# Kernel tuning notes

Hardware: AMD Instinct MI355X
Metric: run time of the kernel (lower is better)

The kernel has to match this reference:

```python
import jax, jax.numpy as jnp
import numpy as np
from jax import lax

N = 4096      # nodes
D = 256       # in_channels
H = 128       # hidden_size (cell output = 2*H = 256)
BLOCK = 128   # row-block size for the masked-max scan
THR = 0.99    # adjacency threshold on uniform A -> avg degree ~41
EPS = 1e-12


def _block_max(m, scores):
    # m: [BLOCK, N] bool, scores: [N, H] -> [BLOCK, H]
    v = jnp.where(m[:, :, None], scores[None, :, :], -jnp.inf)
    return v.max(axis=1)

_block_max = jax.checkpoint(_block_max)


def masked_max(mask, scores):
    # maxpool over neighbors, blocked over destination nodes to avoid an [N,N,H] temp
    n = mask.shape[0]
    mblk = mask.reshape(n // BLOCK, BLOCK, n)
    def body(_, m):
        return None, _block_max(m, scores)
    _, out = lax.scan(body, None, mblk)
    out = out.reshape(n, scores.shape[-1])
    # nodes with no neighbors -> 0
    return jnp.where(jnp.isneginf(out), jnp.zeros_like(out), out)


def setup_inputs() -> dict:
    key = jax.random.key(0)
    ks = jax.random.split(key, 16)
    def w(k, shape):
        fan = shape[0]
        return (jax.random.normal(k, shape, jnp.float32) / np.sqrt(fan)).astype(jnp.float32)
    D1 = 2 * H  # layer-1 input dim (= 256)
    return dict(
        x=jax.random.normal(ks[0], (N, D), jnp.float32),
        A=jax.random.uniform(ks[1], (N, N), dtype=jnp.float32),
        # layer 0 cell params
        Wp0=w(ks[2], (D, H)), bp0=jnp.zeros((H,), jnp.float32),
        Ws0=w(ks[3], (D, H)), bs0=jnp.zeros((H,), jnp.float32),
        Wn0=w(ks[4], (H, H)), bn0=jnp.zeros((H,), jnp.float32),
        # layer 1 cell params
        Wp1=w(ks[5], (D1, H)), bp1=jnp.zeros((H,), jnp.float32),
        Ws1=w(ks[6], (D1, H)), bs1=jnp.zeros((H,), jnp.float32),
        Wn1=w(ks[7], (H, H)), bn1=jnp.zeros((H,), jnp.float32),
    )


def _cell(x, mask, Wp, bp, Ws, bs, Wn, bn):
    # GraphSAGE maxpool cell: concat(self transform, neighbor maxpool transform)
    scores = jax.nn.relu(x @ Wp + bp)                 # [N, H]
    pooled = masked_max(mask, scores)                 # [N, H]
    return jnp.concatenate([x @ Ws + bs, pooled @ Wn + bn], axis=-1)  # [N, 2H]


def reference(x, A, Wp0, bp0, Ws0, bs0, Wn0, bn0, Wp1, bp1, Ws1, bs1, Wn1, bn1):
    mask = A > THR  # [N, N] bool adjacency
    for (Wp, bp, Ws, bs, Wn, bn) in ((Wp0, bp0, Ws0, bs0, Wn0, bn0),
                                     (Wp1, bp1, Ws1, bs1, Wn1, bn1)):
        x = _cell(x, mask, Wp, bp, Ws, bs, Wn, bn)
        x = jax.nn.relu(x)
        nrm = jnp.linalg.norm(x, axis=-1, keepdims=True)
        x = x / jnp.maximum(nrm, EPS)
    return x
```

## Files before the change

kernel.cpp:

```cpp
#include <hip/hip_runtime.h>

#define NN 4096
#define CAP 256
#define THRV 0.99f
#define SROWS 8

typedef __attribute__((ext_vector_type(8))) short short8v;
typedef __attribute__((ext_vector_type(4))) float f32x4;

__device__ inline unsigned short f2bf(float f) {
  unsigned u = __builtin_bit_cast(unsigned, f);
  u = (u + 0x7fffu + ((u >> 16) & 1u)) >> 16;
  return (unsigned short)u;
}
__device__ inline unsigned pkmax(unsigned a, unsigned b) {
  unsigned r;
  asm("v_pk_max_u16 %0, %1, %2" : "=v"(r) : "v"(a), "v"(b));
  return r;
}
__device__ inline uint4 max4(uint4 a, uint4 b) {
  return make_uint4(pkmax(a.x, b.x), pkmax(a.y, b.y), pkmax(a.z, b.z), pkmax(a.w, b.w));
}


__global__ __launch_bounds__(256) void k_scan(
    const float* __restrict__ A, int* __restrict__ cnt, unsigned short* __restrict__ nbr) {
  __shared__ int scnt[SROWS];
  __shared__ unsigned short snb[SROWS][CAP];
  const int tid = threadIdx.x;
  const int lane = tid & 63;
  const int r0 = blockIdx.x * SROWS;
  if (tid < SROWS) scnt[tid] = 0;
  __syncthreads();
  const float4* Arow = (const float4*)(A + (size_t)r0 * NN);
  float4 c0 = Arow[tid], c1 = Arow[tid + 256], c2 = Arow[tid + 512], c3 = Arow[tid + 768];
  for (int r = 0; r < SROWS; ++r) {
    float4 n0 = c0, n1 = c1, n2 = c2, n3 = c3;
    if (r < SROWS - 1) {
      const float4* nx = Arow + (size_t)(r + 1) * (NN / 4);
      n0 = nx[tid]; n1 = nx[tid + 256]; n2 = nx[tid + 512]; n3 = nx[tid + 768];
    }
    unsigned m = 0;
    m |= (c0.x > THRV) ? 0x1u : 0u;    m |= (c0.y > THRV) ? 0x2u : 0u;
    m |= (c0.z > THRV) ? 0x4u : 0u;    m |= (c0.w > THRV) ? 0x8u : 0u;
    m |= (c1.x > THRV) ? 0x10u : 0u;   m |= (c1.y > THRV) ? 0x20u : 0u;
    m |= (c1.z > THRV) ? 0x40u : 0u;   m |= (c1.w > THRV) ? 0x80u : 0u;
    m |= (c2.x > THRV) ? 0x100u : 0u;  m |= (c2.y > THRV) ? 0x200u : 0u;
    m |= (c2.z > THRV) ? 0x400u : 0u;  m |= (c2.w > THRV) ? 0x800u : 0u;
    m |= (c3.x > THRV) ? 0x1000u : 0u; m |= (c3.y > THRV) ? 0x2000u : 0u;
    m |= (c3.z > THRV) ? 0x4000u : 0u; m |= (c3.w > THRV) ? 0x8000u : 0u;
    int cntT = __popc(m);
    int inc = cntT;
#pragma unroll
    for (int off = 1; off < 64; off <<= 1) {
      int o = __shfl_up(inc, off, 64);
      if (lane >= off) inc += o;
    }
    int excl = inc - cntT;
    int wtot = __shfl(inc, 63, 64);
    int wbase = 0;
    if (lane == 0) wbase = atomicAdd(&scnt[r], wtot);
    wbase = __shfl(wbase, 0, 64);
    int pos = wbase + excl;
    while (m) {
      int b = __ffs(m) - 1;
      m &= m - 1;
      if (pos < CAP) snb[r][pos] = (unsigned short)(4 * tid + 1024 * (b >> 2) + (b & 3));
      ++pos;
    }
    c0 = n0; c1 = n1; c2 = n2; c3 = n3;
  }
  __syncthreads();
  if (tid < SROWS) cnt[r0 + tid] = min(scnt[tid], CAP);
  {
    ushort4* dst = (ushort4*)(nbr + (size_t)r0 * CAP);
    const ushort4* s = (const ushort4*)snb;
    dst[tid] = s[tid];
    dst[tid + 256] = s[tid + 256];
  }
}

__global__ __launch_bounds__(256) void k_gp(
    const float* __restrict__ x,
    const float* __restrict__ Wp0, const float* __restrict__ bp0,
    const float* __restrict__ Ws0, const float* __restrict__ bs0,
    const float* __restrict__ Wn0, const float* __restrict__ Wp1,
    const float* __restrict__ Ws1, const float* __restrict__ Wn1,
    unsigned short* __restrict__ scores0, float* __restrict__ S0,
    unsigned short* __restrict__ tWn0, unsigned short* __restrict__ tWp1,
    unsigned short* __restrict__ tWs1, unsigned short* __restrict__ tWn1) {
  __shared__ unsigned short smw[32768];
  const int bid = blockIdx.x;
  const int tid = threadIdx.x;

  if (bid < 128) {
    const int set = bid >> 6;
    const float* W = set ? Ws0 : Wp0;
    const float* bias = set ? bs0 : bp0;
#pragma unroll
    for (int it = 0; it < 32; ++it) {
      int e0 = it * 1024 + tid * 4;
      float4 v = *(const float4*)(W + e0);
      int k = e0 >> 7, n = e0 & 127;
      int elem = (k & 3) + 4 * ((k >> 4) & 1);
      int gg = (k >> 2) & 3;
      int kt8 = (k >> 5) * 8;
      float vv[4] = {v.x, v.y, v.z, v.w};
#pragma unroll
      for (int i = 0; i < 4; ++i) {
        int nn = n + i;
        smw[((kt8 + (nn >> 4)) << 9) + ((gg * 16 + (nn & 15)) << 3) + elem] = f2bf(vv[i]);
      }
    }
    __syncthreads();
    const int wv = tid >> 6, lane = tid & 63;
    const int g = lane >> 4, r15 = lane & 15;
    const int rb16 = (bid & 63) * 64 + wv * 16;
    const int row = rb16 + r15;
    f32x4 acc[8] = {};
#pragma unroll
    for (int ktIdx = 0; ktIdx < 8; ++ktIdx) {
      const float* xp = x + (size_t)row * 256 + ktIdx * 32 + 4 * g;
      float4 lo = *(const float4*)xp;
      float4 hi = *(const float4*)(xp + 16);
      short8v a;
      a[0] = (short)f2bf(lo.x); a[1] = (short)f2bf(lo.y);
      a[2] = (short)f2bf(lo.z); a[3] = (short)f2bf(lo.w);
      a[4] = (short)f2bf(hi.x); a[5] = (short)f2bf(hi.y);
      a[6] = (short)f2bf(hi.z); a[7] = (short)f2bf(hi.w);
#pragma unroll
      for (int nf = 0; nf < 8; ++nf) {
        uint4 bw = *(const uint4*)(smw + ((ktIdx * 8 + nf) << 9) + lane * 8);
        acc[nf] = __builtin_amdgcn_mfma_f32_16x16x32_bf16(a, __builtin_bit_cast(short8v, bw), acc[nf], 0, 0, 0);
      }
    }
#pragma unroll
    for (int nf = 0; nf < 8; ++nf) {
      int col = nf * 16 + r15;
      float bv = bias[col];
#pragma unroll
      for (int r = 0; r < 4; ++r) {
        int orow = rb16 + 4 * g + r;
        float t = acc[nf][r] + bv;
        if (set == 0) scores0[(size_t)orow * 128 + col] = f2bf(fmaxf(t, 0.f));
        else          S0[(size_t)orow * 128 + col] = t;
      }
    }
    return;
  }
  int id = bid - 128;
  const float* src; unsigned short* dst; int base;
  if (id < 16)      { src = Wn0; dst = tWn0; base = id; }
  else if (id < 48) { src = Wp1; dst = tWp1; base = id - 16; }
  else if (id < 80) { src = Ws1; dst = tWs1; base = id - 48; }
  else              { src = Wn1; dst = tWn1; base = id - 80; }
  int e0 = base * 1024 + tid * 4;
  float4 v = *(const float4*)(src + e0);
  int k = e0 >> 7, n = e0 & 127;
  float vv[4] = {v.x, v.y, v.z, v.w};
  int elem = (k & 3) + 4 * ((k >> 4) & 1);
  int gg = (k >> 2) & 3;
  int fragkt = (k >> 5) * 8;
#pragma unroll
  for (int i = 0; i < 4; ++i) {
    int nn = n + i;
    int idx = ((fragkt + (nn >> 4)) << 9) + ((gg * 16 + (nn & 15)) << 3) + elem;
    dst[idx] = f2bf(vv[i]);
  }
}

template<int LAYER>
__global__ __launch_bounds__(512) void fusedL(
    const int* __restrict__ cnt, const unsigned short* __restrict__ nbr,
    const unsigned short* __restrict__ scores_in, const float* __restrict__ S_in,
    const unsigned short* __restrict__ tWn, const float* __restrict__ bn,
    const unsigned short* __restrict__ tWp, const float* __restrict__ bp,
    const unsigned short* __restrict__ tWs, const float* __restrict__ bs,
    unsigned short* __restrict__ scores_out, float* __restrict__ S_out,
    float* __restrict__ out) {
  __shared__ int scnt[16];
  __shared__ unsigned short snb[16][CAP];
  __shared__ unsigned short pool2[16][2][136];
  __shared__ unsigned short pooled[16][136];
  __shared__ unsigned short xb[16][264];
  __shared__ float ssqs[16];
  __shared__ float ssqw[4][16];

  const int tid = threadIdx.x;
  const int wv = tid >> 6, lane = tid & 63, g = lane >> 4, r15 = lane & 15;
  const int r0 = blockIdx.x * 16;

  if (tid < 16) scnt[tid] = cnt[r0 + tid];
  {
    const ushort4* src = (const ushort4*)(nbr + (size_t)r0 * CAP);
    ushort4* dst = (ushort4*)snb;
    dst[tid] = src[tid];
    dst[tid + 512] = src[tid + 512];
  }
  __syncthreads();

  {
    const int r = tid >> 5, sub = tid & 31;
    const int h = sub >> 4, c8 = (sub & 15) * 8;
    const int c = scnt[r];
    uint4 m0 = make_uint4(0, 0, 0, 0), m1 = m0, m2 = m0, m3 = m0;
    int k = h;
    for (; k + 6 < c; k += 8) {
      int j0 = snb[r][k], j1 = snb[r][k + 2], j2 = snb[r][k + 4], j3 = snb[r][k + 6];
      uint4 a0 = *(const uint4*)(scores_in + (size_t)j0 * 128 + c8);
      uint4 a1 = *(const uint4*)(scores_in + (size_t)j1 * 128 + c8);
      uint4 a2 = *(const uint4*)(scores_in + (size_t)j2 * 128 + c8);
      uint4 a3 = *(const uint4*)(scores_in + (size_t)j3 * 128 + c8);
      m0 = max4(m0, a0); m1 = max4(m1, a1); m2 = max4(m2, a2); m3 = max4(m3, a3);
    }
    for (; k < c; k += 2)
      m0 = max4(m0, *(const uint4*)(scores_in + (size_t)snb[r][k] * 128 + c8));
    *(uint4*)&pool2[r][h][c8] = max4(max4(m0, m1), max4(m2, m3));
  }
  __syncthreads();
  if (tid < 256) {
    const int r = tid >> 4, c8 = (tid & 15) * 8;
    uint4 a = *(const uint4*)&pool2[r][0][c8];
    uint4 b = *(const uint4*)&pool2[r][1][c8];
    *(uint4*)&pooled[r][c8] = max4(a, b);
  }
  __syncthreads();

  float sv[8];
  f32x4 pacc[2] = {};
  const int srow = tid >> 4, sc8 = (tid & 15) * 8;
  if (tid < 256) {
    const float* sp = S_in + (size_t)(r0 + srow) * 128 + sc8;
    float4 sa = *(const float4*)sp;
    float4 sb = *(const float4*)(sp + 4);
    sv[0] = fmaxf(sa.x, 0.f); sv[1] = fmaxf(sa.y, 0.f);
    sv[2] = fmaxf(sa.z, 0.f); sv[3] = fmaxf(sa.w, 0.f);
    sv[4] = fmaxf(sb.x, 0.f); sv[5] = fmaxf(sb.y, 0.f);
    sv[6] = fmaxf(sb.z, 0.f); sv[7] = fmaxf(sb.w, 0.f);
    float ps = 0.f;
#pragma unroll
    for (int i = 0; i < 8; ++i) ps += sv[i] * sv[i];
#pragma unroll
    for (int off = 1; off < 16; off <<= 1) ps += __shfl_xor(ps, off, 16);
    if ((tid & 15) == 0) ssqs[srow] = ps;
  } else {
    const int wv2 = wv - 4;
#pragma unroll
    for (int kt = 0; kt < 128; kt += 32) {
      ushort4 alo = *(const ushort4*)&pooled[r15][kt + 4 * g];
      ushort4 ahi = *(const ushort4*)&pooled[r15][kt + 16 + 4 * g];
      short8v a;
      a[0] = alo.x; a[1] = alo.y; a[2] = alo.z; a[3] = alo.w;
      a[4] = ahi.x; a[5] = ahi.y; a[6] = ahi.z; a[7] = ahi.w;
#pragma unroll
      for (int f = 0; f < 2; ++f) {
        uint4 bw = *((const uint4*)(tWn + (size_t)((kt >> 5) * 8 + 2 * wv2 + f) * 512) + lane);
        pacc[f] = __builtin_amdgcn_mfma_f32_16x16x32_bf16(a, __builtin_bit_cast(short8v, bw), pacc[f], 0, 0, 0);
      }
    }
#pragma unroll
    for (int f = 0; f < 2; ++f) {
      float bv = bn[(2 * wv2 + f) * 16 + r15];
#pragma unroll
      for (int rr = 0; rr < 4; ++rr) pacc[f][rr] = fmaxf(pacc[f][rr] + bv, 0.f);
    }
#pragma unroll
    for (int rr = 0; rr < 4; ++rr) {
      float ps = pacc[0][rr] * pacc[0][rr] + pacc[1][rr] * pacc[1][rr];
#pragma unroll
      for (int off = 1; off < 16; off <<= 1) ps += __shfl_xor(ps, off, 16);
      if (r15 == 0) ssqw[wv2][4 * g + rr] = ps;
    }
  }
  __syncthreads();

  if (LAYER == 0) {
    if (tid < 256) {
      float tot = ssqs[srow] + ssqw[0][srow] + ssqw[1][srow] + ssqw[2][srow] + ssqw[3][srow];
      float sc = 1.f / fmaxf(sqrtf(tot), 1e-12f);
      unsigned short hh[8];
#pragma unroll
      for (int i = 0; i < 8; ++i) hh[i] = f2bf(sv[i] * sc);
      uint4 wvv;
      wvv.x = (unsigned)hh[0] | ((unsigned)hh[1] << 16);
      wvv.y = (unsigned)hh[2] | ((unsigned)hh[3] << 16);
      wvv.z = (unsigned)hh[4] | ((unsigned)hh[5] << 16);
      wvv.w = (unsigned)hh[6] | ((unsigned)hh[7] << 16);
      *(uint4*)&xb[srow][sc8] = wvv;
    } else {
      const int wv2 = wv - 4;
#pragma unroll
      for (int rr = 0; rr < 4; ++rr) {
        int row = 4 * g + rr;
        float tot = ssqs[row] + ssqw[0][row] + ssqw[1][row] + ssqw[2][row] + ssqw[3][row];
        float sc = 1.f / fmaxf(sqrtf(tot), 1e-12f);
#pragma unroll
        for (int f = 0; f < 2; ++f)
          xb[row][128 + (2 * wv2 + f) * 16 + r15] = f2bf(pacc[f][rr] * sc);
      }
    }
    __syncthreads();
    const int s = wv >> 2;
    const unsigned short* Wt = s ? tWs : tWp;
    const float* bb = s ? bs : bp;
    const int nf0 = (wv & 3) * 2;
    f32x4 dacc[2] = {};
#pragma unroll
    for (int kt = 0; kt < 256; kt += 32) {
      ushort4 alo = *(const ushort4*)&xb[r15][kt + 4 * g];
      ushort4 ahi = *(const ushort4*)&xb[r15][kt + 16 + 4 * g];
      short8v a;
      a[0] = alo.x; a[1] = alo.y; a[2] = alo.z; a[3] = alo.w;
      a[4] = ahi.x; a[5] = ahi.y; a[6] = ahi.z; a[7] = ahi.w;
#pragma unroll
      for (int f = 0; f < 2; ++f) {
        uint4 bw = *((const uint4*)(Wt + (size_t)((kt >> 5) * 8 + nf0 + f) * 512) + lane);
        dacc[f] = __builtin_amdgcn_mfma_f32_16x16x32_bf16(a, __builtin_bit_cast(short8v, bw), dacc[f], 0, 0, 0);
      }
    }
#pragma unroll
    for (int f = 0; f < 2; ++f) {
      int col = (nf0 + f) * 16 + r15;
      float bv = bb[col];
#pragma unroll
      for (int rr = 0; rr < 4; ++rr) {
        int grow = r0 + 4 * g + rr;
        float t = dacc[f][rr] + bv;
        if (s == 0) scores_out[(size_t)grow * 128 + col] = f2bf(fmaxf(t, 0.f));
        else        S_out[(size_t)grow * 128 + col] = t;
      }
    }
  } else {
    if (tid < 256) {
      float tot = ssqs[srow] + ssqw[0][srow] + ssqw[1][srow] + ssqw[2][srow] + ssqw[3][srow];
      float sc = 1.f / fmaxf(sqrtf(tot), 1e-12f);
      float* op = out + (size_t)(r0 + srow) * 256 + sc8;
      *(float4*)op = make_float4(sv[0] * sc, sv[1] * sc, sv[2] * sc, sv[3] * sc);
      *(float4*)(op + 4) = make_float4(sv[4] * sc, sv[5] * sc, sv[6] * sc, sv[7] * sc);
    } else {
      const int wv2 = wv - 4;
#pragma unroll
      for (int rr = 0; rr < 4; ++rr) {
        int row = 4 * g + rr;
        float tot = ssqs[row] + ssqw[0][row] + ssqw[1][row] + ssqw[2][row] + ssqw[3][row];
        float sc = 1.f / fmaxf(sqrtf(tot), 1e-12f);
#pragma unroll
        for (int f = 0; f < 2; ++f)
          out[(size_t)(r0 + row) * 256 + 128 + (2 * wv2 + f) * 16 + r15] = pacc[f][rr] * sc;
      }
    }
  }
}

extern "C" void kernel_launch(void* const* d_in, const int* in_sizes, int n_in,
                              void* d_out, int out_size, void* d_ws, size_t ws_size,
                              hipStream_t stream) {
  (void)in_sizes; (void)n_in; (void)out_size; (void)ws_size;
  const float* x   = (const float*)d_in[0];
  const float* A   = (const float*)d_in[1];
  const float* Wp0 = (const float*)d_in[2];
  const float* bp0 = (const float*)d_in[3];
  const float* Ws0 = (const float*)d_in[4];
  const float* bs0 = (const float*)d_in[5];
  const float* Wn0 = (const float*)d_in[6];
  const float* bn0 = (const float*)d_in[7];
  const float* Wp1 = (const float*)d_in[8];
  const float* bp1 = (const float*)d_in[9];
  const float* Ws1 = (const float*)d_in[10];
  const float* bs1 = (const float*)d_in[11];
  const float* Wn1 = (const float*)d_in[12];
  const float* bn1 = (const float*)d_in[13];

  char* ws = (char*)d_ws;
  auto alloc = [&](size_t bytes) { char* p = ws; ws += (bytes + 255) & ~(size_t)255; return p; };
  int* cnt             = (int*)alloc((size_t)NN * 4);
  unsigned short* nbr  = (unsigned short*)alloc((size_t)NN * CAP * 2);
  unsigned short* tWn0 = (unsigned short*)alloc(128 * 128 * 2);
  unsigned short* tWp1 = (unsigned short*)alloc(256 * 128 * 2);
  unsigned short* tWs1 = (unsigned short*)alloc(256 * 128 * 2);
  unsigned short* tWn1 = (unsigned short*)alloc(128 * 128 * 2);
  unsigned short* scores0 = (unsigned short*)alloc((size_t)NN * 128 * 2);
  unsigned short* scores1 = (unsigned short*)alloc((size_t)NN * 128 * 2);
  float* S0            = (float*)alloc((size_t)NN * 128 * 4);
  float* S1            = (float*)alloc((size_t)NN * 128 * 4);

  k_scan<<<NN / SROWS, 256, 0, stream>>>(A, cnt, nbr);
  k_gp<<<224, 256, 0, stream>>>(x, Wp0, bp0, Ws0, bs0, Wn0, Wp1, Ws1, Wn1,
                                scores0, S0, tWn0, tWp1, tWs1, tWn1);
  fusedL<0><<<NN / 16, 512, 0, stream>>>(cnt, nbr, scores0, S0,
                                         tWn0, bn0, tWp1, bp1, tWs1, bs1,
                                         scores1, S1, nullptr);
  fusedL<1><<<NN / 16, 512, 0, stream>>>(cnt, nbr, scores1, S1,
                                         tWn1, bn1, nullptr, nullptr, nullptr, nullptr,
                                         nullptr, nullptr, (float*)d_out);
}
```

Baseline: 50.78 us.

## Fuse adjacency threshold scan into layer-0 fused kernel

Removes the separate k_scan kernel and builds each block's neighbor lists directly in fusedL<0>, with 512 threads scanning the block's 16 rows of A. The neighbor list is built in shared memory and written out for reuse by layer 1. This drops one kernel launch and the round trip of neighbor lists through global memory for layer 0. The cost is that the 64MB scan of A now runs with only 256 blocks of 512 threads, so A bandwidth may be harder to saturate, and it is serialized inside the layer-0 kernel.

New measurement: 50.02 us. Within noise of the previous version (-1.5%).

```diff
diff --git a/kernel.cpp b/kernel.cpp
--- a/kernel.cpp
+++ b/kernel.cpp
@@ -3,7 +3,6 @@
 #define NN 4096
 #define CAP 256
 #define THRV 0.99f
-#define SROWS 8
 
 typedef __attribute__((ext_vector_type(8))) short short8v;
 typedef __attribute__((ext_vector_type(4))) float f32x4;
@@ -22,63 +21,6 @@
   return make_uint4(pkmax(a.x, b.x), pkmax(a.y, b.y), pkmax(a.z, b.z), pkmax(a.w, b.w));
 }
 
-
-__global__ __launch_bounds__(256) void k_scan(
-    const float* __restrict__ A, int* __restrict__ cnt, unsigned short* __restrict__ nbr) {
-  __shared__ int scnt[SROWS];
-  __shared__ unsigned short snb[SROWS][CAP];
-  const int tid = threadIdx.x;
-  const int lane = tid & 63;
-  const int r0 = blockIdx.x * SROWS;
-  if (tid < SROWS) scnt[tid] = 0;
-  __syncthreads();
-  const float4* Arow = (const float4*)(A + (size_t)r0 * NN);
-  float4 c0 = Arow[tid], c1 = Arow[tid + 256], c2 = Arow[tid + 512], c3 = Arow[tid + 768];
-  for (int r = 0; r < SROWS; ++r) {
-    float4 n0 = c0, n1 = c1, n2 = c2, n3 = c3;
-    if (r < SROWS - 1) {
-      const float4* nx = Arow + (size_t)(r + 1) * (NN / 4);
-      n0 = nx[tid]; n1 = nx[tid + 256]; n2 = nx[tid + 512]; n3 = nx[tid + 768];
-    }
-    unsigned m = 0;
-    m |= (c0.x > THRV) ? 0x1u : 0u;    m |= (c0.y > THRV) ? 0x2u : 0u;
-    m |= (c0.z > THRV) ? 0x4u : 0u;    m |= (c0.w > THRV) ? 0x8u : 0u;
-    m |= (c1.x > THRV) ? 0x10u : 0u;   m |= (c1.y > THRV) ? 0x20u : 0u;
-    m |= (c1.z > THRV) ? 0x40u : 0u;   m |= (c1.w > THRV) ? 0x80u : 0u;
-    m |= (c2.x > THRV) ? 0x100u : 0u;  m |= (c2.y > THRV) ? 0x200u : 0u;
-    m |= (c2.z > THRV) ? 0x400u : 0u;  m |= (c2.w > THRV) ? 0x800u : 0u;
-    m |= (c3.x > THRV) ? 0x1000u : 0u; m |= (c3.y > THRV) ? 0x2000u : 0u;
-    m |= (c3.z > THRV) ? 0x4000u : 0u; m |= (c3.w > THRV) ? 0x8000u : 0u;
-    int cntT = __popc(m);
-    int inc = cntT;
-#pragma unroll
-    for (int off = 1; off < 64; off <<= 1) {
-      int o = __shfl_up(inc, off, 64);
-      if (lane >= off) inc += o;
-    }
-    int excl = inc - cntT;
-    int wtot = __shfl(inc, 63, 64);
-    int wbase = 0;
-    if (lane == 0) wbase = atomicAdd(&scnt[r], wtot);
-    wbase = __shfl(wbase, 0, 64);
-    int pos = wbase + excl;
-    while (m) {
-      int b = __ffs(m) - 1;
-      m &= m - 1;
-      if (pos < CAP) snb[r][pos] = (unsigned short)(4 * tid + 1024 * (b >> 2) + (b & 3));
-      ++pos;
-    }
-    c0 = n0; c1 = n1; c2 = n2; c3 = n3;
-  }
-  __syncthreads();
-  if (tid < SROWS) cnt[r0 + tid] = min(scnt[tid], CAP);
-  {
-    ushort4* dst = (ushort4*)(nbr + (size_t)r0 * CAP);
-    const ushort4* s = (const ushort4*)snb;
-    dst[tid] = s[tid];
-    dst[tid + 256] = s[tid + 256];
-  }
-}
 
 __global__ __launch_bounds__(256) void k_gp(
     const float* __restrict__ x,
@@ -171,7 +113,8 @@
 
 template<int LAYER>
 __global__ __launch_bounds__(512) void fusedL(
-    const int* __restrict__ cnt, const unsigned short* __restrict__ nbr,
+    const float* __restrict__ A,
+    int* __restrict__ cnt, unsigned short* __restrict__ nbr,
     const unsigned short* __restrict__ scores_in, const float* __restrict__ S_in,
     const unsigned short* __restrict__ tWn, const float* __restrict__ bn,
     const unsigned short* __restrict__ tWp, const float* __restrict__ bp,
@@ -190,14 +133,62 @@
   const int wv = tid >> 6, lane = tid & 63, g = lane >> 4, r15 = lane & 15;
   const int r0 = blockIdx.x * 16;
 
-  if (tid < 16) scnt[tid] = cnt[r0 + tid];
-  {
-    const ushort4* src = (const ushort4*)(nbr + (size_t)r0 * CAP);
-    ushort4* dst = (ushort4*)snb;
-    dst[tid] = src[tid];
-    dst[tid + 512] = src[tid + 512];
-  }
-  __syncthreads();
+  if (LAYER == 0) {
+    if (tid < 16) scnt[tid] = 0;
+    __syncthreads();
+    const float4* Ar = (const float4*)(A + (size_t)r0 * NN);
+    float4 c0 = Ar[tid], c1 = Ar[tid + 512];
+    for (int r = 0; r < 16; ++r) {
+      float4 n0 = c0, n1 = c1;
+      if (r < 15) {
+        const float4* nx = Ar + (size_t)(r + 1) * (NN / 4);
+        n0 = nx[tid]; n1 = nx[tid + 512];
+      }
+      unsigned m = 0;
+      m |= (c0.x > THRV) ? 0x1u : 0u;  m |= (c0.y > THRV) ? 0x2u : 0u;
+      m |= (c0.z > THRV) ? 0x4u : 0u;  m |= (c0.w > THRV) ? 0x8u : 0u;
+      m |= (c1.x > THRV) ? 0x10u : 0u; m |= (c1.y > THRV) ? 0x20u : 0u;
+      m |= (c1.z > THRV) ? 0x40u : 0u; m |= (c1.w > THRV) ? 0x80u : 0u;
+      int cntT = __popc(m);
+      int inc = cntT;
+#pragma unroll
+      for (int off = 1; off < 64; off <<= 1) {
+        int o = __shfl_up(inc, off, 64);
+        if (lane >= off) inc += o;
+      }
+      int excl = inc - cntT;
+      int wtot = __shfl(inc, 63, 64);
+      int wbase = 0;
+      if (lane == 0) wbase = atomicAdd(&scnt[r], wtot);
+      wbase = __shfl(wbase, 0, 64);
+      int pos = wbase + excl;
+      while (m) {
+        int b = __ffs(m) - 1;
+        m &= m - 1;
+        if (pos < CAP) snb[r][pos] = (unsigned short)(4 * tid + 2048 * (b >> 2) + (b & 3));
+        ++pos;
+      }
+      c0 = n0; c1 = n1;
+    }
+    __syncthreads();
+    if (tid < 16) { int c = min(scnt[tid], CAP); scnt[tid] = c; cnt[r0 + tid] = c; }
+    __syncthreads();
+    {
+      ushort4* dst = (ushort4*)(nbr + (size_t)r0 * CAP);
+      const ushort4* s = (const ushort4*)snb;
+      dst[tid] = s[tid];
+      dst[tid + 512] = s[tid + 512];
+    }
+  } else {
+    if (tid < 16) scnt[tid] = cnt[r0 + tid];
+    {
+      const ushort4* src = (const ushort4*)(nbr + (size_t)r0 * CAP);
+      ushort4* dst = (ushort4*)snb;
+      dst[tid] = src[tid];
+      dst[tid + 512] = src[tid + 512];
+    }
+    __syncthreads();
+  }
 
   {
     const int r = tid >> 5, sub = tid & 31;
@@ -384,13 +375,12 @@
   float* S0            = (float*)alloc((size_t)NN * 128 * 4);
   float* S1            = (float*)alloc((size_t)NN * 128 * 4);
 
-  k_scan<<<NN / SROWS, 256, 0, stream>>>(A, cnt, nbr);
   k_gp<<<224, 256, 0, stream>>>(x, Wp0, bp0, Ws0, bs0, Wn0, Wp1, Ws1, Wn1,
                                 scores0, S0, tWn0, tWp1, tWs1, tWn1);
-  fusedL<0><<<NN / 16, 512, 0, stream>>>(cnt, nbr, scores0, S0,
+  fusedL<0><<<NN / 16, 512, 0, stream>>>(A, cnt, nbr, scores0, S0,
                                          tWn0, bn0, tWp1, bp1, tWs1, bs1,
                                          scores1, S1, nullptr);
-  fusedL<1><<<NN / 16, 512, 0, stream>>>(cnt, nbr, scores1, S1,
+  fusedL<1><<<NN / 16, 512, 0, stream>>>(A, cnt, nbr, scores1, S1,
                                          tWn1, bn1, nullptr, nullptr, nullptr, nullptr,
                                          nullptr, nullptr, (float*)d_out);
 }
```
